# Kernel optimization log

Measured on AMD Instinct MI355X. Metric: run time of the kernel, lower is better.

## Reference

```python
import jax, jax.numpy as jnp
import numpy as np

N_QUBITS = 12
DIM = 2 ** N_QUBITS
N_RES_LAYERS = 3
N_HEADS = 2
N_ATTN_LAYERS = 2
SEQ_LEN = 64
HORIZON = 4
BATCH = 8
N_PARAMS = N_QUBITS * 2 * N_ATTN_LAYERS  # 48
FEAT = N_QUBITS * N_HEADS  # 24

# ---- static (numpy) precomputed gate structures (little-endian, qiskit convention) ----
_idx = np.arange(DIM)

def _cx_perm(c, t):
    # CNOT: flip target bit where control bit is 1 -> index permutation
    return np.where(((_idx >> c) & 1) == 1, _idx ^ (1 << t), _idx)

def _cz_phase(a, b):
    return (1.0 - 2.0 * (((_idx >> a) & 1) * ((_idx >> b) & 1))).astype(np.float32)

CX_LADDER = [jnp.asarray(_cx_perm(i, i + 1)) for i in range(N_QUBITS - 1)]
CX_RING = jnp.asarray(_cx_perm(N_QUBITS - 1, 0))
CX_LONG = jnp.asarray(_cx_perm(0, N_QUBITS - 1))
_CZ = []
for _layer in range(N_RES_LAYERS):
    _ph = np.ones(DIM, np.float32)
    for _i in range(_layer % 2, N_QUBITS - 1, 2):
        _ph *= _cz_phase(_i, _i + 1)
    _CZ.append(jnp.asarray(_ph))
# Qiskit Pauli label 'I'*i + 'Z' + 'I'*(n-i-1) acts on qubit n-1-i (big-endian labels)
Z_SIGNS = jnp.asarray(np.stack([
    (1.0 - 2.0 * ((_idx >> (N_QUBITS - 1 - i)) & 1)).astype(np.float32)
    for i in range(N_QUBITS)]))  # (n, DIM)


def _apply_1q(state, gate, q):
    # state: (..., DIM); gate: (2,2) or (...,2,2) broadcastable against leading dims
    hi = DIM >> (q + 1)
    lo = 1 << q
    s = state.reshape(state.shape[:-1] + (hi, 2, lo))
    out = jnp.einsum('...ij,...hjl->...hil', gate, s)
    return out.reshape(state.shape)


def _ry(theta):
    c = jnp.cos(theta / 2)
    s = jnp.sin(theta / 2)
    g = jnp.stack([jnp.stack([c, -s], -1), jnp.stack([s, c], -1)], -2)
    return g.astype(jnp.complex64)


def _rz(phi):
    em = jnp.exp(-0.5j * phi)
    ep = jnp.exp(0.5j * phi)
    z = jnp.zeros_like(em)
    return jnp.stack([jnp.stack([em, z], -1), jnp.stack([z, ep], -1)], -2)


def _u3(t, p, l):
    ct = jnp.cos(t / 2).astype(jnp.complex64)
    st = jnp.sin(t / 2).astype(jnp.complex64)
    return jnp.stack([jnp.stack([ct, -jnp.exp(1j * l) * st]),
                      jnp.stack([jnp.exp(1j * p) * st, jnp.exp(1j * (p + l)) * ct])])


def _encode_reservoir(x, res_params):
    # x: (B,T) normalized scalars -> batched statevectors (B,T,DIM)
    B, T = x.shape
    # H^{\otimes n} |0...0> = uniform superposition
    state = jnp.full((B, T, DIM), 1.0 / np.sqrt(DIM), jnp.complex64)
    for i in range(N_QUBITS):
        state = _apply_1q(state, _ry(x * np.pi * (i + 1) / N_QUBITS), i)
        state = _apply_1q(state, _rz(x * np.pi / (i + 1)), i)
    for p in CX_LADDER:
        state = state[..., p]
    state = state[..., CX_RING]
    # fixed random reservoir
    for layer in range(N_RES_LAYERS):
        for i in range(N_QUBITS):
            g = _u3(res_params[layer, i, 0], res_params[layer, i, 1], res_params[layer, i, 2])
            state = _apply_1q(state, g, i)
        state = state * _CZ[layer]
        state = state[..., CX_LONG]  # n > 2
    return state


def _project(state, params):
    # projection circuit: per layer RY/RZ on each qubit then CNOT ladder; then <Z_i>
    for layer in range(N_ATTN_LAYERS):
        for i in range(N_QUBITS):
            k = (layer * N_QUBITS + i) * 2
            state = _apply_1q(state, _ry(params[k]), i)
            state = _apply_1q(state, _rz(params[k + 1]), i)
        for p in CX_LADDER:
            state = state[..., p]
    probs = state.real ** 2 + state.imag ** 2  # (B,T,DIM)
    return jnp.einsum('btd,qd->btq', probs, Z_SIGNS)  # (B,T,n)


def setup_inputs() -> dict:
    key = jax.random.key(0)
    ks = jax.random.split(key, 6)
    sequence = jax.random.uniform(ks[0], (BATCH, SEQ_LEN), jnp.float32)
    res_params = jax.random.uniform(ks[1], (N_RES_LAYERS, N_QUBITS, 3), jnp.float32,
                                    minval=0.0, maxval=2.0 * np.pi)
    head_params = jax.random.uniform(ks[2], (N_HEADS, 3, N_PARAMS), jnp.float32,
                                     minval=0.0, maxval=2.0 * np.pi)
    W1 = jax.random.normal(ks[3], (FEAT, 2 * FEAT), jnp.float32) / np.sqrt(FEAT)
    b1 = jnp.zeros((2 * FEAT,), jnp.float32)
    W2 = jax.random.normal(ks[4], (2 * FEAT, HORIZON), jnp.float32) / np.sqrt(2 * FEAT)
    b2 = jnp.zeros((HORIZON,), jnp.float32)
    return {'sequence': sequence, 'res_params': res_params, 'head_params': head_params,
            'W1': W1, 'b1': b1, 'W2': W2, 'b2': b2}


def reference(sequence, res_params, head_params, W1, b1, W2, b2):
    states = _encode_reservoir(sequence, res_params)  # (B,T,DIM)
    T = sequence.shape[1]
    mask = jnp.triu(jnp.full((T, T), -1e9, jnp.float32), k=1)
    outs = []
    for h in range(N_HEADS):
        Q = _project(states, head_params[h, 0])
        K = _project(states, head_params[h, 1])
        V = _project(states, head_params[h, 2])
        scores = jnp.einsum('btd,bsd->bts', Q, K) / np.sqrt(N_QUBITS) + mask
        attn = jax.nn.softmax(scores, axis=-1)
        outs.append(jnp.einsum('bts,bsd->btd', attn, V))
    feats = jnp.concatenate(outs, -1)  # (B,T,FEAT)
    last = feats[:, -1, :]
    hdn = jax.nn.gelu(last @ W1 + b1, approximate=False)  # torch GELU default = exact erf
    pred = hdn @ W2 + b2  # (B, HORIZON)
    return pred
```

## Files before the change

### kernel.cpp

```cpp
#include <hip/hip_runtime.h>
#include <hip/hip_bf16.h>


#define PADDED 4224

__device__ __forceinline__ int PD(int j) { return j + (j >> 5); }

__device__ __forceinline__ int mapIdx(int j, int mode) {
  if (mode == 1) { int k = j ^ ((j >> 11) & 1); return k ^ ((k & 0x7FF) << 1); }
  if (mode == 2) { return j ^ ((j & 1) << 11); }
  if (mode == 3) { return j ^ ((j & 0x7FF) << 1); }
  return j;
}

template <int L>
__device__ __forceinline__ int layoutIdx(int tid, int r) {
  if constexpr (L == 0) return (tid << 4) | r;
  else if constexpr (L == 1) return ((tid & 0xF0) << 4) | (r << 4) | (tid & 15);
  else return (r << 8) | tid;
}

template <int L>
__device__ __forceinline__ void ldsRead16(const float* sR, const float* sI, int tid, int mode,
                                          float ar[16], float ai[16]) {
#pragma unroll
  for (int r = 0; r < 16; ++r) {
    int j = layoutIdx<L>(tid, r);
    int a = PD(mapIdx(j, mode));
    ar[r] = sR[a]; ai[r] = sI[a];
  }
}

template <int L>
__device__ __forceinline__ void ldsWrite16(float* sR, float* sI, int tid,
                                           const float ar[16], const float ai[16], int czmask) {
#pragma unroll
  for (int r = 0; r < 16; ++r) {
    int j = layoutIdx<L>(tid, r);
    float vr = ar[r], vi = ai[r];
    if (czmask) {
      float sg = (__popc((j & (j >> 1)) & czmask) & 1) ? -1.0f : 1.0f;
      vr *= sg; vi *= sg;
    }
    int a = PD(j);
    sR[a] = vr; sI[a] = vi;
  }
}

__device__ __forceinline__ void applyU34(float ar[16], float ai[16], const float (*ut)[8]) {
#pragma unroll
  for (int b = 0; b < 4; ++b) {
    const float* u = ut[b];
    float u00r = u[0];
    float u01r = u[2], u01i = u[3];
    float u10r = u[4], u10i = u[5], u11r = u[6], u11i = u[7];
#pragma unroll
    for (int m = 0; m < 8; ++m) {
      int p0 = ((m >> b) << (b + 1)) | (m & ((1 << b) - 1));
      int p1 = p0 | (1 << b);
      float x0r = ar[p0], x0i = ai[p0], x1r = ar[p1], x1i = ai[p1];
      ar[p0] = u00r * x0r + u01r * x1r - u01i * x1i;
      ai[p0] = u00r * x0i + u01r * x1i + u01i * x1r;
      ar[p1] = u10r * x0r - u10i * x0i + u11r * x1r - u11i * x1i;
      ai[p1] = u10r * x0i + u10i * x0r + u11r * x1i + u11i * x1r;
    }
  }
}

__device__ __forceinline__ void applyRyRz4(float ar[16], float ai[16], const float4* gt) {
#pragma unroll
  for (int b = 0; b < 4; ++b) {
    float4 g = gt[b];
    float c = g.x, s = g.y, zr = g.z, zi = g.w;
#pragma unroll
    for (int m = 0; m < 8; ++m) {
      int p0 = ((m >> b) << (b + 1)) | (m & ((1 << b) - 1));
      int p1 = p0 | (1 << b);
      float x0r = ar[p0], x0i = ai[p0], x1r = ar[p1], x1i = ai[p1];
      float n0r = c * x0r - s * x1r;
      float n0i = c * x0i - s * x1i;
      float wr  = s * x0r + c * x1r;
      float wi  = s * x0i + c * x1i;
      ar[p0] = n0r;              ai[p0] = n0i;
      ar[p1] = wr * zr - wi * zi; ai[p1] = wr * zi + wi * zr;
    }
  }
}

template <int L>
__device__ __forceinline__ void encPass(float* sR, float* sI, int tid, int mode,
                                        const float (*ut)[8], int czmask) {
  float ar[16], ai[16];
  ldsRead16<L>(sR, sI, tid, mode, ar, ai);
  if (mode != 0) __syncthreads();
  applyU34(ar, ai, ut);
  ldsWrite16<L>(sR, sI, tid, ar, ai, czmask);
  __syncthreads();
}

template <int L>
__device__ __forceinline__ void projPass(float* sR, float* sI, int tid, int mode, const float4* gt) {
  float ar[16], ai[16];
  ldsRead16<L>(sR, sI, tid, mode, ar, ai);
  if (mode != 0) __syncthreads();
  applyRyRz4(ar, ai, gt);
  ldsWrite16<L>(sR, sI, tid, ar, ai, 0);
  __syncthreads();
}

__device__ __forceinline__ void projFinal(const float* sR, const float* sI, int tid,
                                          const float4* gt, float feat[12]) {
  float ar[16], ai[16];
#pragma unroll
  for (int r = 0; r < 16; ++r) {
    int a = PD((r << 8) | tid);
    ar[r] = sR[a]; ai[r] = sI[a];
  }
  applyRyRz4(ar, ai, gt);
  float sp = 0.f, f0 = 0.f, f1 = 0.f, f2 = 0.f, f3 = 0.f;
  int pt = __popc(tid) & 1;
#pragma unroll
  for (int r = 0; r < 16; ++r) {
    float p = ar[r] * ar[r] + ai[r] * ai[r];
    sp += p;
    int tr = r ^ (r << 1); tr ^= (tr << 2);
    f0 += ((pt ^ ((tr >> 3) & 1)) ? -p : p);
    f1 += ((pt ^ ((tr >> 2) & 1)) ? -p : p);
    f2 += ((pt ^ ((tr >> 1) & 1)) ? -p : p);
    f3 += ((pt ^ (tr & 1)) ? -p : p);
  }
  feat[0] = f0; feat[1] = f1; feat[2] = f2; feat[3] = f3;
  int tt = tid ^ (tid << 1); tt ^= (tt << 2); tt ^= (tt << 4);
#pragma unroll
  for (int q = 4; q < 12; ++q)
    feat[q] = ((tt >> (11 - q)) & 1) ? -sp : sp;
}

__device__ __forceinline__ float waveReduce(float v) {
#pragma unroll
  for (int off = 32; off; off >>= 1) v += __shfl_xor(v, off, 64);
  return v;
}


__device__ __forceinline__ void buildQtab(float4* qtab, int tid, float x) {
  const float PI = 3.14159265358979323846f;
  const float RS2 = 0.70710678118654752440f;
  if (tid < 12) {
    int i = tid;
    float th = x * PI * (float)(i + 1) / 12.0f;
    float ph = x * PI / (float)(i + 1);
    float s, c;  sincosf(0.5f * th, &s, &c);
    float zi, zr; sincosf(0.5f * ph, &zi, &zr);
    float k0 = (c - s) * RS2, k1 = (c + s) * RS2;
    qtab[i] = make_float4(k0 * zr, -k0 * zi, k1 * zr, k1 * zi);
  }
}

__device__ __forceinline__ void buildUtab(float (*utab)[8], int tid, const float* resp) {
  if (tid >= 64 && tid < 100) {
    int i = tid - 64;
    const float* rp = resp + i * 3;
    float st, ct;  sincosf(0.5f * rp[0], &st, &ct);
    float sp2, cp; sincosf(rp[1], &sp2, &cp);
    float sl, cl;  sincosf(rp[2], &sl, &cl);
    float spl, cpl; sincosf(rp[1] + rp[2], &spl, &cpl);
    float* u = utab[i];
    u[0] = ct;       u[1] = 0.0f;
    u[2] = -cl * st; u[3] = -sl * st;
    u[4] = cp * st;  u[5] = sp2 * st;
    u[6] = cpl * ct; u[7] = spl * ct;
  }
}

__device__ __forceinline__ void initProduct(float* sRe, float* sIm, int tid, const float4* qtab) {
  float pr, pi;
  {
    float4 g = qtab[4];
    int sb = tid & 1;
    pr = sb ? g.z : g.x; pi = sb ? g.w : g.y;
  }
#pragma unroll
  for (int q = 5; q < 12; ++q) {
    float4 g = qtab[q];
    int sb = (tid >> (q - 4)) & 1;
    float fr = sb ? g.z : g.x, fi = sb ? g.w : g.y;
    float nr = pr * fr - pi * fi;
    pi = pr * fi + pi * fr; pr = nr;
  }
  float4 g0 = qtab[0], g1 = qtab[1], g2 = qtab[2], g3 = qtab[3];
  float c01r[4], c01i[4], c23r[4], c23i[4];
#pragma unroll
  for (int i2 = 0; i2 < 4; ++i2) {
    float f0r = (i2 & 1) ? g0.z : g0.x, f0i = (i2 & 1) ? g0.w : g0.y;
    float f1r = (i2 & 2) ? g1.z : g1.x, f1i = (i2 & 2) ? g1.w : g1.y;
    c01r[i2] = f0r * f1r - f0i * f1i; c01i[i2] = f0r * f1i + f0i * f1r;
    float f2r = (i2 & 1) ? g2.z : g2.x, f2i = (i2 & 1) ? g2.w : g2.y;
    float f3r = (i2 & 2) ? g3.z : g3.x, f3i = (i2 & 2) ? g3.w : g3.y;
    c23r[i2] = f2r * f3r - f2i * f3i; c23i[i2] = f2r * f3i + f2i * f3r;
  }
#pragma unroll
  for (int r = 0; r < 16; ++r) {
    float lr = c01r[r & 3] * c23r[r >> 2] - c01i[r & 3] * c23i[r >> 2];
    float li = c01r[r & 3] * c23i[r >> 2] + c01i[r & 3] * c23r[r >> 2];
    int a = PD((tid << 4) | r);
    sRe[a] = pr * lr - pi * li;
    sIm[a] = pr * li + pi * lr;
  }
}

__device__ __forceinline__ void buildPtab(float4* ptab, int tid, const float* hp) {
  if (tid < 24) {
    int k = tid * 2;
    float s, c;  sincosf(0.5f * hp[k], &s, &c);
    float zi, zr; sincosf(hp[k + 1], &zi, &zr);
    ptab[tid] = make_float4(c, s, zr, zi);
  }
}


__global__ __launch_bounds__(256, 2) void enc_kernel(
    const float* __restrict__ seq, const float* __restrict__ resp,
    float* __restrict__ wsStates) {
  __shared__ float sRe[PADDED], sIm[PADDED];
  __shared__ float4 qtab[12];
  __shared__ float utab[36][8];

  const int tid = threadIdx.x;
  const int blk = blockIdx.x;
  const float x = seq[blk];

  buildQtab(qtab, tid, x);
  buildUtab(utab, tid, resp);
  __syncthreads();

  initProduct(sRe, sIm, tid, qtab);
  __syncthreads();

  encPass<0>(sRe, sIm, tid, 1, &utab[0], 0);
  encPass<1>(sRe, sIm, tid, 0, &utab[4], 0);
  encPass<2>(sRe, sIm, tid, 0, &utab[8], 0x555);
  encPass<0>(sRe, sIm, tid, 2, &utab[12], 0);
  encPass<1>(sRe, sIm, tid, 0, &utab[16], 0);
  encPass<2>(sRe, sIm, tid, 0, &utab[20], 0x2AA);
  encPass<0>(sRe, sIm, tid, 2, &utab[24], 0);
  encPass<1>(sRe, sIm, tid, 0, &utab[28], 0);

  {
    float ar[16], ai[16];
    ldsRead16<2>(sRe, sIm, tid, 0, ar, ai);
    applyU34(ar, ai, &utab[32]);
    float* gR = wsStates + (size_t)blk * 8192;
    float* gI = gR + 4096;
#pragma unroll
    for (int r = 0; r < 16; ++r) {
      int j = (r << 8) | tid;
      float sg = (__popc((j & (j >> 1)) & 0x555) & 1) ? -1.0f : 1.0f;
      int g = j ^ ((j & 1) << 11);
      gR[g] = sg * ar[r];
      gI[g] = sg * ai[r];
    }
  }
}

__global__ __launch_bounds__(256, 4) void proj_kernel(
    const float* __restrict__ wsStates, const float* __restrict__ hparams,
    float* __restrict__ featBase) {
  __shared__ float sRe[PADDED], sIm[PADDED];
  __shared__ float4 ptab[24];
  __shared__ float red[4][12];

  const int tid = threadIdx.x;
  const int bid = blockIdx.x;
  int h, which, s;
  if (bid < 2048) { s = bid >> 2; int pp = bid & 3; h = pp >> 1; which = 1 + (pp & 1); }
  else            { int i = bid - 2048; h = i & 1; s = (((i >> 1) << 6) | 63); which = 0; }
  const int b = s >> 6, t = s & 63;

  buildPtab(ptab, tid, hparams + (h * 3 + which) * 48);

  float ar[16], ai[16];
  const float4* pR = (const float4*)(wsStates + (size_t)s * 8192 + (tid << 4));
  const float4* pI = (const float4*)(wsStates + (size_t)s * 8192 + 4096 + (tid << 4));
#pragma unroll
  for (int k = 0; k < 4; ++k) {
    float4 vr = pR[k], vi = pI[k];
    ar[4 * k] = vr.x; ar[4 * k + 1] = vr.y; ar[4 * k + 2] = vr.z; ar[4 * k + 3] = vr.w;
    ai[4 * k] = vi.x; ai[4 * k + 1] = vi.y; ai[4 * k + 2] = vi.z; ai[4 * k + 3] = vi.w;
  }
  __syncthreads();

  applyRyRz4(ar, ai, &ptab[0]);
  ldsWrite16<0>(sRe, sIm, tid, ar, ai, 0);
  __syncthreads();

  projPass<1>(sRe, sIm, tid, 0, &ptab[4]);
  projPass<2>(sRe, sIm, tid, 0, &ptab[8]);
  projPass<0>(sRe, sIm, tid, 3, &ptab[12]);
  projPass<1>(sRe, sIm, tid, 0, &ptab[16]);

  float feat[12];
  projFinal(sRe, sIm, tid, &ptab[20], feat);
#pragma unroll
  for (int q = 0; q < 12; ++q) feat[q] = waveReduce(feat[q]);
  int wid = tid >> 6;
  if ((tid & 63) == 0) {
#pragma unroll
    for (int q = 0; q < 12; ++q) red[wid][q] = feat[q];
  }
  __syncthreads();
  if (tid < 12) {
    float v = red[0][tid] + red[1][tid] + red[2][tid] + red[3][tid];
    float* dst;
    if (which == 1)      dst = featBase + (((h << 3) + b) * 64 + t) * 12;
    else if (which == 2) dst = featBase + 12288 + (((h << 3) + b) * 64 + t) * 12;
    else                 dst = featBase + 24576 + ((h << 3) + b) * 12;
    dst[tid] = v;
  }
}


__global__ __launch_bounds__(256, 2) void qstates_mono(
    const float* __restrict__ seq, const float* __restrict__ resp,
    const float* __restrict__ hparams, float* __restrict__ featBase) {
  __shared__ float sRe[PADDED], sIm[PADDED];
  __shared__ float4 qtab[12];
  __shared__ float utab[36][8];
  __shared__ float4 ptab[24];
  __shared__ float red[4][12];

  const int tid = threadIdx.x;
  const int blk = blockIdx.x;
  const int b = blk >> 6;
  const int t = blk & 63;
  const float x = seq[blk];

  buildQtab(qtab, tid, x);
  buildUtab(utab, tid, resp);
  __syncthreads();
  initProduct(sRe, sIm, tid, qtab);
  __syncthreads();

  for (int l = 0; l < 3; ++l) {
    int czm = (l & 1) ? 0x2AA : 0x555;
    encPass<0>(sRe, sIm, tid, (l == 0) ? 1 : 2, &utab[l * 12], 0);
    encPass<1>(sRe, sIm, tid, 0, &utab[l * 12 + 4], 0);
    encPass<2>(sRe, sIm, tid, 0, &utab[l * 12 + 8], czm);
  }

  float encR[16], encI[16];
#pragma unroll
  for (int r = 0; r < 16; ++r) {
    int j = (tid << 4) | r;
    int a = PD(j ^ ((j & 1) << 11));
    encR[r] = sRe[a]; encI[r] = sIm[a];
  }

  const int nproj = (t == 63) ? 6 : 4;
  for (int pj = 0; pj < nproj; ++pj) {
    int h, which;
    if (pj < 4) { h = pj >> 1; which = (pj & 1) ? 2 : 1; }
    else        { h = pj - 4;  which = 0; }
    buildPtab(ptab, tid, hparams + (h * 3 + which) * 48);
    __syncthreads();

    float ar[16], ai[16];
#pragma unroll
    for (int r = 0; r < 16; ++r) { ar[r] = encR[r]; ai[r] = encI[r]; }
    applyRyRz4(ar, ai, &ptab[0]);
    ldsWrite16<0>(sRe, sIm, tid, ar, ai, 0);
    __syncthreads();
    projPass<1>(sRe, sIm, tid, 0, &ptab[4]);
    projPass<2>(sRe, sIm, tid, 0, &ptab[8]);
    projPass<0>(sRe, sIm, tid, 3, &ptab[12]);
    projPass<1>(sRe, sIm, tid, 0, &ptab[16]);

    float feat[12];
    projFinal(sRe, sIm, tid, &ptab[20], feat);
#pragma unroll
    for (int q = 0; q < 12; ++q) feat[q] = waveReduce(feat[q]);
    int wid = tid >> 6;
    if ((tid & 63) == 0) {
#pragma unroll
      for (int q = 0; q < 12; ++q) red[wid][q] = feat[q];
    }
    __syncthreads();
    if (tid < 12) {
      float v = red[0][tid] + red[1][tid] + red[2][tid] + red[3][tid];
      float* dst;
      if (which == 1)      dst = featBase + (((h << 3) + b) * 64 + t) * 12;
      else if (which == 2) dst = featBase + 12288 + (((h << 3) + b) * 64 + t) * 12;
      else                 dst = featBase + 24576 + ((h << 3) + b) * 12;
      dst[tid] = v;
    }
    __syncthreads();
  }
}


__global__ __launch_bounds__(64) void qhead_kernel(
    const float* __restrict__ featBase,
    const float* __restrict__ W1, const float* __restrict__ b1,
    const float* __restrict__ W2, const float* __restrict__ b2,
    float* __restrict__ out) {
  __shared__ float feats[24];
  __shared__ float hdn[48];
  const int b = blockIdx.x;
  const int lane = threadIdx.x;
  const float* Kf = featBase;
  const float* Vf = featBase + 12288;
  const float* Qf = featBase + 24576;
  for (int h = 0; h < 2; ++h) {
    const float* q  = Qf + ((h << 3) + b) * 12;
    const float* kr = Kf + ((((h << 3) + b) << 6) + lane) * 12;
    float dot = 0.f;
#pragma unroll
    for (int d = 0; d < 12; ++d) dot += q[d] * kr[d];
    dot *= 0.288675134594812882f;
    float mx = dot;
#pragma unroll
    for (int off = 32; off; off >>= 1) mx = fmaxf(mx, __shfl_xor(mx, off, 64));
    float e = expf(dot - mx);
    float se = e;
#pragma unroll
    for (int off = 32; off; off >>= 1) se += __shfl_xor(se, off, 64);
    float a = e / se;
    const float* vr = Vf + ((((h << 3) + b) << 6) + lane) * 12;
#pragma unroll
    for (int d = 0; d < 12; ++d) {
      float v = a * vr[d];
#pragma unroll
      for (int off = 32; off; off >>= 1) v += __shfl_xor(v, off, 64);
      if (lane == 0) feats[h * 12 + d] = v;
    }
  }
  __syncthreads();
  if (lane < 48) {
    float acc = b1[lane];
#pragma unroll
    for (int f = 0; f < 24; ++f) acc += feats[f] * W1[f * 48 + lane];
    hdn[lane] = 0.5f * acc * (1.0f + erff(acc * 0.70710678118654752440f));
  }
  __syncthreads();
  if (lane < 4) {
    float acc = b2[lane];
#pragma unroll
    for (int k = 0; k < 48; ++k) acc += hdn[k] * W2[k * 4 + lane];
    out[(b << 2) | lane] = acc;
  }
}

extern "C" void kernel_launch(void* const* d_in, const int* in_sizes, int n_in,
                              void* d_out, int out_size, void* d_ws, size_t ws_size,
                              hipStream_t stream) {
  const float* seq     = (const float*)d_in[0];
  const float* resp    = (const float*)d_in[1];
  const float* hparams = (const float*)d_in[2];
  const float* W1      = (const float*)d_in[3];
  const float* b1      = (const float*)d_in[4];
  const float* W2      = (const float*)d_in[5];
  const float* b2      = (const float*)d_in[6];
  float* out = (float*)d_out;
  float* ws  = (float*)d_ws;

  const size_t needSplit = ((size_t)512 * 8192 + 24768) * sizeof(float);
  if (ws_size >= needSplit) {
    float* wsStates = ws;
    float* featBase = ws + (size_t)512 * 8192;
    hipLaunchKernelGGL(enc_kernel, dim3(512), dim3(256), 0, stream, seq, resp, wsStates);
    hipLaunchKernelGGL(proj_kernel, dim3(2064), dim3(256), 0, stream, wsStates, hparams, featBase);
    hipLaunchKernelGGL(qhead_kernel, dim3(8), dim3(64), 0, stream, featBase, W1, b1, W2, b2, out);
  } else {
    hipLaunchKernelGGL(qstates_mono, dim3(512), dim3(256), 0, stream, seq, resp, hparams, ws);
    hipLaunchKernelGGL(qhead_kernel, dim3(8), dim3(64), 0, stream, ws, W1, b1, W2, b2, out);
  }
}
```

Baseline: 147.9 us.

## Keep projection state in registers with single-buffer LDS permutes and precomputed gate tables

```diff
diff --git a/kernel.cpp b/kernel.cpp
--- a/kernel.cpp
+++ b/kernel.cpp
@@ -2,35 +2,37 @@
 #include <hip/hip_bf16.h>
 
 
+#define N_STATE_F (512 * 8192)
+#define WS_FEAT   N_STATE_F
+#define WS_PTAB   (WS_FEAT + 24768)
+#define WS_TOTAL  (WS_PTAB + 576)
+
+#define ENC_PI 3.14159265358979323846f
+#define ENC_RS2 0.70710678118654752440f
+
 #define PADDED 4224
-
 __device__ __forceinline__ int PD(int j) { return j + (j >> 5); }
-
 __device__ __forceinline__ int mapIdx(int j, int mode) {
   if (mode == 1) { int k = j ^ ((j >> 11) & 1); return k ^ ((k & 0x7FF) << 1); }
   if (mode == 2) { return j ^ ((j & 1) << 11); }
   if (mode == 3) { return j ^ ((j & 0x7FF) << 1); }
   return j;
 }
-
 template <int L>
 __device__ __forceinline__ int layoutIdx(int tid, int r) {
   if constexpr (L == 0) return (tid << 4) | r;
   else if constexpr (L == 1) return ((tid & 0xF0) << 4) | (r << 4) | (tid & 15);
   else return (r << 8) | tid;
 }
-
 template <int L>
 __device__ __forceinline__ void ldsRead16(const float* sR, const float* sI, int tid, int mode,
                                           float ar[16], float ai[16]) {
 #pragma unroll
   for (int r = 0; r < 16; ++r) {
-    int j = layoutIdx<L>(tid, r);
-    int a = PD(mapIdx(j, mode));
+    int a = PD(mapIdx(layoutIdx<L>(tid, r), mode));
     ar[r] = sR[a]; ai[r] = sI[a];
   }
 }
-
 template <int L>
 __device__ __forceinline__ void ldsWrite16(float* sR, float* sI, int tid,
                                            const float ar[16], const float ai[16], int czmask) {
@@ -46,13 +48,11 @@
     sR[a] = vr; sI[a] = vi;
   }
 }
-
 __device__ __forceinline__ void applyU34(float ar[16], float ai[16], const float (*ut)[8]) {
 #pragma unroll
   for (int b = 0; b < 4; ++b) {
     const float* u = ut[b];
-    float u00r = u[0];
-    float u01r = u[2], u01i = u[3];
+    float u00r = u[0], u01r = u[2], u01i = u[3];
     float u10r = u[4], u10i = u[5], u11r = u[6], u11i = u[7];
 #pragma unroll
     for (int m = 0; m < 8; ++m) {
@@ -66,7 +66,6 @@
     }
   }
 }
-
 __device__ __forceinline__ void applyRyRz4(float ar[16], float ai[16], const float4* gt) {
 #pragma unroll
   for (int b = 0; b < 4; ++b) {
@@ -81,12 +80,11 @@
       float n0i = c * x0i - s * x1i;
       float wr  = s * x0r + c * x1r;
       float wi  = s * x0i + c * x1i;
-      ar[p0] = n0r;              ai[p0] = n0i;
+      ar[p0] = n0r;               ai[p0] = n0i;
       ar[p1] = wr * zr - wi * zi; ai[p1] = wr * zi + wi * zr;
     }
   }
 }
-
 template <int L>
 __device__ __forceinline__ void encPass(float* sR, float* sI, int tid, int mode,
                                         const float (*ut)[8], int czmask) {
@@ -97,66 +95,21 @@
   ldsWrite16<L>(sR, sI, tid, ar, ai, czmask);
   __syncthreads();
 }
-
-template <int L>
-__device__ __forceinline__ void projPass(float* sR, float* sI, int tid, int mode, const float4* gt) {
-  float ar[16], ai[16];
-  ldsRead16<L>(sR, sI, tid, mode, ar, ai);
-  if (mode != 0) __syncthreads();
-  applyRyRz4(ar, ai, gt);
-  ldsWrite16<L>(sR, sI, tid, ar, ai, 0);
-  __syncthreads();
-}
-
-__device__ __forceinline__ void projFinal(const float* sR, const float* sI, int tid,
-                                          const float4* gt, float feat[12]) {
-  float ar[16], ai[16];
-#pragma unroll
-  for (int r = 0; r < 16; ++r) {
-    int a = PD((r << 8) | tid);
-    ar[r] = sR[a]; ai[r] = sI[a];
-  }
-  applyRyRz4(ar, ai, gt);
-  float sp = 0.f, f0 = 0.f, f1 = 0.f, f2 = 0.f, f3 = 0.f;
-  int pt = __popc(tid) & 1;
-#pragma unroll
-  for (int r = 0; r < 16; ++r) {
-    float p = ar[r] * ar[r] + ai[r] * ai[r];
-    sp += p;
-    int tr = r ^ (r << 1); tr ^= (tr << 2);
-    f0 += ((pt ^ ((tr >> 3) & 1)) ? -p : p);
-    f1 += ((pt ^ ((tr >> 2) & 1)) ? -p : p);
-    f2 += ((pt ^ ((tr >> 1) & 1)) ? -p : p);
-    f3 += ((pt ^ (tr & 1)) ? -p : p);
-  }
-  feat[0] = f0; feat[1] = f1; feat[2] = f2; feat[3] = f3;
-  int tt = tid ^ (tid << 1); tt ^= (tt << 2); tt ^= (tt << 4);
-#pragma unroll
-  for (int q = 4; q < 12; ++q)
-    feat[q] = ((tt >> (11 - q)) & 1) ? -sp : sp;
-}
-
 __device__ __forceinline__ float waveReduce(float v) {
 #pragma unroll
   for (int off = 32; off; off >>= 1) v += __shfl_xor(v, off, 64);
   return v;
 }
-
-
 __device__ __forceinline__ void buildQtab(float4* qtab, int tid, float x) {
-  const float PI = 3.14159265358979323846f;
-  const float RS2 = 0.70710678118654752440f;
   if (tid < 12) {
-    int i = tid;
-    float th = x * PI * (float)(i + 1) / 12.0f;
-    float ph = x * PI / (float)(i + 1);
+    float th = x * ENC_PI * (float)(tid + 1) / 12.0f;
+    float ph = x * ENC_PI / (float)(tid + 1);
     float s, c;  sincosf(0.5f * th, &s, &c);
     float zi, zr; sincosf(0.5f * ph, &zi, &zr);
-    float k0 = (c - s) * RS2, k1 = (c + s) * RS2;
-    qtab[i] = make_float4(k0 * zr, -k0 * zi, k1 * zr, k1 * zi);
-  }
-}
-
+    float k0 = (c - s) * ENC_RS2, k1 = (c + s) * ENC_RS2;
+    qtab[tid] = make_float4(k0 * zr, -k0 * zi, k1 * zr, k1 * zi);
+  }
+}
 __device__ __forceinline__ void buildUtab(float (*utab)[8], int tid, const float* resp) {
   if (tid >= 64 && tid < 100) {
     int i = tid - 64;
@@ -172,14 +125,9 @@
     u[6] = cpl * ct; u[7] = spl * ct;
   }
 }
-
 __device__ __forceinline__ void initProduct(float* sRe, float* sIm, int tid, const float4* qtab) {
   float pr, pi;
-  {
-    float4 g = qtab[4];
-    int sb = tid & 1;
-    pr = sb ? g.z : g.x; pi = sb ? g.w : g.y;
-  }
+  { float4 g = qtab[4]; int sb = tid & 1; pr = sb ? g.z : g.x; pi = sb ? g.w : g.y; }
 #pragma unroll
   for (int q = 5; q < 12; ++q) {
     float4 g = qtab[q];
@@ -208,7 +156,6 @@
     sIm[a] = pr * li + pi * lr;
   }
 }
-
 __device__ __forceinline__ void buildPtab(float4* ptab, int tid, const float* hp) {
   if (tid < 24) {
     int k = tid * 2;
@@ -218,6 +165,17 @@
   }
 }
 
+__global__ void prep_kernel(const float* __restrict__ hparams, float* __restrict__ ws) {
+  int t = threadIdx.x;
+  float4* ptab = (float4*)(ws + WS_PTAB);
+  for (int idx = t; idx < 144; idx += 256) {
+    int pj = idx / 24, k = idx % 24;
+    const float* hp = hparams + pj * 48;
+    float s, c;  sincosf(0.5f * hp[2 * k], &s, &c);
+    float zi, zr; sincosf(hp[2 * k + 1], &zi, &zr);
+    ptab[idx] = make_float4(c, s, zr, zi);
+  }
+}
 
 __global__ __launch_bounds__(256, 2) void enc_kernel(
     const float* __restrict__ seq, const float* __restrict__ resp,
@@ -263,10 +221,27 @@
   }
 }
 
-__global__ __launch_bounds__(256, 4) void proj_kernel(
-    const float* __restrict__ wsStates, const float* __restrict__ hparams,
+template <int W, int R>
+__device__ __forceinline__ void perm16(float* M, int tid, int map,
+                                       float (&ar)[16], float (&ai)[16]) {
+#pragma unroll
+  for (int r = 0; r < 16; ++r) M[PD(layoutIdx<W>(tid, r))] = ai[r];
+  __syncthreads();
+#pragma unroll
+  for (int r = 0; r < 16; ++r) ai[r] = M[PD(mapIdx(layoutIdx<R>(tid, r), map))];
+  __syncthreads();
+#pragma unroll
+  for (int r = 0; r < 16; ++r) M[PD(layoutIdx<W>(tid, r))] = ar[r];
+  __syncthreads();
+#pragma unroll
+  for (int r = 0; r < 16; ++r) ar[r] = M[PD(mapIdx(layoutIdx<R>(tid, r), map))];
+  __syncthreads();
+}
+
+__global__ __launch_bounds__(256, 8) void proj_kernel(
+    const float* __restrict__ wsStates, const float* __restrict__ ptabG,
     float* __restrict__ featBase) {
-  __shared__ float sRe[PADDED], sIm[PADDED];
+  __shared__ float M[PADDED];
   __shared__ float4 ptab[24];
   __shared__ float red[4][12];
 
@@ -277,7 +252,7 @@
   else            { int i = bid - 2048; h = i & 1; s = (((i >> 1) << 6) | 63); which = 0; }
   const int b = s >> 6, t = s & 63;
 
-  buildPtab(ptab, tid, hparams + (h * 3 + which) * 48);
+  if (tid < 24) ptab[tid] = ((const float4*)ptabG)[(h * 3 + which) * 24 + tid];
 
   float ar[16], ai[16];
   const float4* pR = (const float4*)(wsStates + (size_t)s * 8192 + (tid << 4));
@@ -291,16 +266,36 @@
   __syncthreads();
 
   applyRyRz4(ar, ai, &ptab[0]);
-  ldsWrite16<0>(sRe, sIm, tid, ar, ai, 0);
-  __syncthreads();
-
-  projPass<1>(sRe, sIm, tid, 0, &ptab[4]);
-  projPass<2>(sRe, sIm, tid, 0, &ptab[8]);
-  projPass<0>(sRe, sIm, tid, 3, &ptab[12]);
-  projPass<1>(sRe, sIm, tid, 0, &ptab[16]);
-
+  perm16<0, 1>(M, tid, 0, ar, ai);
+  applyRyRz4(ar, ai, &ptab[4]);
+  perm16<1, 2>(M, tid, 0, ar, ai);
+  applyRyRz4(ar, ai, &ptab[8]);
+  perm16<2, 0>(M, tid, 3, ar, ai);
+  applyRyRz4(ar, ai, &ptab[12]);
+  perm16<0, 1>(M, tid, 0, ar, ai);
+  applyRyRz4(ar, ai, &ptab[16]);
+  perm16<1, 2>(M, tid, 0, ar, ai);
+  applyRyRz4(ar, ai, &ptab[20]);
+
+  float sp = 0.f, f0 = 0.f, f1 = 0.f, f2 = 0.f, f3 = 0.f;
+  int pt = __popc(tid) & 1;
+#pragma unroll
+  for (int r = 0; r < 16; ++r) {
+    float p = ar[r] * ar[r] + ai[r] * ai[r];
+    sp += p;
+    int tr = r ^ (r << 1); tr ^= (tr << 2);
+    f0 += ((pt ^ ((tr >> 3) & 1)) ? -p : p);
+    f1 += ((pt ^ ((tr >> 2) & 1)) ? -p : p);
+    f2 += ((pt ^ ((tr >> 1) & 1)) ? -p : p);
+    f3 += ((pt ^ (tr & 1)) ? -p : p);
+  }
   float feat[12];
-  projFinal(sRe, sIm, tid, &ptab[20], feat);
+  feat[0] = f0; feat[1] = f1; feat[2] = f2; feat[3] = f3;
+  int tt = tid ^ (tid << 1); tt ^= (tt << 2); tt ^= (tt << 4);
+#pragma unroll
+  for (int q = 4; q < 12; ++q)
+    feat[q] = ((tt >> (11 - q)) & 1) ? -sp : sp;
+
 #pragma unroll
   for (int q = 0; q < 12; ++q) feat[q] = waveReduce(feat[q]);
   int wid = tid >> 6;
@@ -319,7 +314,42 @@
   }
 }
 
-
+template <int L>
+__device__ __forceinline__ void projPassM(float* sR, float* sI, int tid, int mode, const float4* gt) {
+  float ar[16], ai[16];
+  ldsRead16<L>(sR, sI, tid, mode, ar, ai);
+  if (mode != 0) __syncthreads();
+  applyRyRz4(ar, ai, gt);
+  ldsWrite16<L>(sR, sI, tid, ar, ai, 0);
+  __syncthreads();
+}
+__device__ __forceinline__ void projFinalM(const float* sR, const float* sI, int tid,
+                                           const float4* gt, float feat[12]) {
+  float ar[16], ai[16];
+#pragma unroll
+  for (int r = 0; r < 16; ++r) {
+    int a = PD((r << 8) | tid);
+    ar[r] = sR[a]; ai[r] = sI[a];
+  }
+  applyRyRz4(ar, ai, gt);
+  float sp = 0.f, f0 = 0.f, f1 = 0.f, f2 = 0.f, f3 = 0.f;
+  int pt = __popc(tid) & 1;
+#pragma unroll
+  for (int r = 0; r < 16; ++r) {
+    float p = ar[r] * ar[r] + ai[r] * ai[r];
+    sp += p;
+    int tr = r ^ (r << 1); tr ^= (tr << 2);
+    f0 += ((pt ^ ((tr >> 3) & 1)) ? -p : p);
+    f1 += ((pt ^ ((tr >> 2) & 1)) ? -p : p);
+    f2 += ((pt ^ ((tr >> 1) & 1)) ? -p : p);
+    f3 += ((pt ^ (tr & 1)) ? -p : p);
+  }
+  feat[0] = f0; feat[1] = f1; feat[2] = f2; feat[3] = f3;
+  int tt = tid ^ (tid << 1); tt ^= (tt << 2); tt ^= (tt << 4);
+#pragma unroll
+  for (int q = 4; q < 12; ++q)
+    feat[q] = ((tt >> (11 - q)) & 1) ? -sp : sp;
+}
 __global__ __launch_bounds__(256, 2) void qstates_mono(
     const float* __restrict__ seq, const float* __restrict__ resp,
     const float* __restrict__ hparams, float* __restrict__ featBase) {
@@ -328,26 +358,21 @@
   __shared__ float utab[36][8];
   __shared__ float4 ptab[24];
   __shared__ float red[4][12];
-
   const int tid = threadIdx.x;
   const int blk = blockIdx.x;
-  const int b = blk >> 6;
-  const int t = blk & 63;
+  const int b = blk >> 6, t = blk & 63;
   const float x = seq[blk];
-
   buildQtab(qtab, tid, x);
   buildUtab(utab, tid, resp);
   __syncthreads();
   initProduct(sRe, sIm, tid, qtab);
   __syncthreads();
-
-  for (int l = 0; l < 3; ++l) {
-    int czm = (l & 1) ? 0x2AA : 0x555;
-    encPass<0>(sRe, sIm, tid, (l == 0) ? 1 : 2, &utab[l * 12], 0);
-    encPass<1>(sRe, sIm, tid, 0, &utab[l * 12 + 4], 0);
-    encPass<2>(sRe, sIm, tid, 0, &utab[l * 12 + 8], czm);
-  }
-
+  for (int ly = 0; ly < 3; ++ly) {
+    int czm = (ly & 1) ? 0x2AA : 0x555;
+    encPass<0>(sRe, sIm, tid, (ly == 0) ? 1 : 2, &utab[ly * 12], 0);
+    encPass<1>(sRe, sIm, tid, 0, &utab[ly * 12 + 4], 0);
+    encPass<2>(sRe, sIm, tid, 0, &utab[ly * 12 + 8], czm);
+  }
   float encR[16], encI[16];
 #pragma unroll
   for (int r = 0; r < 16; ++r) {
@@ -355,7 +380,6 @@
     int a = PD(j ^ ((j & 1) << 11));
     encR[r] = sRe[a]; encI[r] = sIm[a];
   }
-
   const int nproj = (t == 63) ? 6 : 4;
   for (int pj = 0; pj < nproj; ++pj) {
     int h, which;
@@ -363,20 +387,18 @@
     else        { h = pj - 4;  which = 0; }
     buildPtab(ptab, tid, hparams + (h * 3 + which) * 48);
     __syncthreads();
-
     float ar[16], ai[16];
 #pragma unroll
     for (int r = 0; r < 16; ++r) { ar[r] = encR[r]; ai[r] = encI[r]; }
     applyRyRz4(ar, ai, &ptab[0]);
     ldsWrite16<0>(sRe, sIm, tid, ar, ai, 0);
     __syncthreads();
-    projPass<1>(sRe, sIm, tid, 0, &ptab[4]);
-    projPass<2>(sRe, sIm, tid, 0, &ptab[8]);
-    projPass<0>(sRe, sIm, tid, 3, &ptab[12]);
-    projPass<1>(sRe, sIm, tid, 0, &ptab[16]);
-
+    projPassM<1>(sRe, sIm, tid, 0, &ptab[4]);
+    projPassM<2>(sRe, sIm, tid, 0, &ptab[8]);
+    projPassM<0>(sRe, sIm, tid, 3, &ptab[12]);
+    projPassM<1>(sRe, sIm, tid, 0, &ptab[16]);
     float feat[12];
-    projFinal(sRe, sIm, tid, &ptab[20], feat);
+    projFinalM(sRe, sIm, tid, &ptab[20], feat);
 #pragma unroll
     for (int q = 0; q < 12; ++q) feat[q] = waveReduce(feat[q]);
     int wid = tid >> 6;
@@ -396,7 +418,6 @@
     __syncthreads();
   }
 }
-
 
 __global__ __launch_bounds__(64) void qhead_kernel(
     const float* __restrict__ featBase,
@@ -463,12 +484,14 @@
   float* out = (float*)d_out;
   float* ws  = (float*)d_ws;
 
-  const size_t needSplit = ((size_t)512 * 8192 + 24768) * sizeof(float);
+  const size_t needSplit = (size_t)WS_TOTAL * sizeof(float);
   if (ws_size >= needSplit) {
     float* wsStates = ws;
-    float* featBase = ws + (size_t)512 * 8192;
+    float* featBase = ws + WS_FEAT;
+    float* ptabG    = ws + WS_PTAB;
+    hipLaunchKernelGGL(prep_kernel, dim3(1), dim3(256), 0, stream, hparams, ws);
     hipLaunchKernelGGL(enc_kernel, dim3(512), dim3(256), 0, stream, seq, resp, wsStates);
-    hipLaunchKernelGGL(proj_kernel, dim3(2064), dim3(256), 0, stream, wsStates, hparams, featBase);
+    hipLaunchKernelGGL(proj_kernel, dim3(2064), dim3(256), 0, stream, wsStates, ptabG, featBase);
     hipLaunchKernelGGL(qhead_kernel, dim3(8), dim3(64), 0, stream, featBase, W1, b1, W2, b2, out);
   } else {
     hipLaunchKernelGGL(qstates_mono, dim3(512), dim3(256), 0, stream, seq, resp, hparams, ws);
```

Measured after the change: 219.1 us. 1.48x slower.
